# Optimization experiments

Measured on AMD Instinct MI355X. Metric: run time of the kernel, lower is better.

## Reference

```python
import jax, jax.numpy as jnp
import numpy as np

N = 50000   # nodes
E = 500000  # edges
DIN = 128
DOUT = 128
H = 8       # mulhead
DH = DOUT // H
L = 2       # layers per branch
NC = 7      # emotion classes
EPS = 1e-9  # BatchNorm eps from source


def _bn(x):
    # BatchNorm1d in train mode, gamma=1/beta=0 at init
    m = x.mean(axis=0)
    v = x.var(axis=0)
    return (x - m) * jax.lax.rsqrt(v + EPS)


def _gat_forward(f, row, col, vals, Ws, bs, Wn, bn, As, An):
    for i in range(L):
        hs = jax.nn.relu(jnp.einsum('nd,hdk->nhk', f, Ws[i]) + bs[i])  # [N,H,DH]
        hn = jax.nn.relu(jnp.einsum('nd,hdk->nhk', f, Wn[i]) + bn[i])  # [N,H,DH]
        ats = jax.nn.leaky_relu(jnp.einsum('nhk,hk->nh', hs, As[i]), negative_slope=0.2)  # [N,H]
        # NOTE: source computes attention_neigh from f_self (faithful)
        atn = jax.nn.leaky_relu(jnp.einsum('nhk,hk->nh', hs, An[i]), negative_slope=0.2)  # [N,H]
        e = (ats[row] + atn[col]) * vals[:, None]            # [E,H] per-edge attention
        msg = e[:, :, None] * hn[col]                        # [E,H,DH] gather + weight
        agg = jax.ops.segment_sum(msg, row, num_segments=N)  # [N,H,DH] scatter-add (sparse mm)
        f = _bn(agg.reshape(N, H * DH))                      # concat heads + norm
    return f


def _gcn_forward(f, row, col, vals, W, b):
    for i in range(L):
        h = f @ W[i] + b[i]                                  # [N,DOUT]
        agg = jax.ops.segment_sum(vals[:, None] * h[col], row, num_segments=N)
        f = _bn(jax.nn.relu(agg))
    return f


def setup_inputs() -> dict:
    key = jax.random.key(0)
    ks = jax.random.split(key, 24)
    inp = {}
    inp['f_in'] = jax.random.normal(ks[0], (N, DIN), jnp.float32)
    inp['edge_row'] = jax.random.randint(ks[1], (E,), 0, N, jnp.int32)
    inp['edge_col'] = jax.random.randint(ks[2], (E,), 0, N, jnp.int32)
    inp['vals_gat'] = jax.random.uniform(ks[3], (E,), jnp.float32)
    inp['vals_uttr'] = jax.random.uniform(ks[4], (E,), jnp.float32)
    inp['vals_past'] = jax.random.uniform(ks[5], (E,), jnp.float32)
    inp['vals_futr'] = jax.random.uniform(ks[6], (E,), jnp.float32)
    s = 0.05
    # GAT params (stacked over [layer, head]); layer0 in=DIN, later in=DOUT (equal here)
    inp['gat_Ws'] = jax.random.normal(ks[7], (L, H, DIN, DH), jnp.float32) * s
    inp['gat_bs'] = jnp.zeros((L, H, DH), jnp.float32)
    inp['gat_Wn'] = jax.random.normal(ks[8], (L, H, DIN, DH), jnp.float32) * s
    inp['gat_bn'] = jnp.zeros((L, H, DH), jnp.float32)
    inp['gat_as'] = jnp.ones((L, H, DH), jnp.float32)  # init ones per source
    inp['gat_an'] = jnp.ones((L, H, DH), jnp.float32)
    # three vanilla GCN branches
    inp['W_uttr'] = jax.random.normal(ks[9], (L, DIN, DOUT), jnp.float32) * s
    inp['b_uttr'] = jnp.zeros((L, DOUT), jnp.float32)
    inp['W_past'] = jax.random.normal(ks[10], (L, DIN, DOUT), jnp.float32) * s
    inp['b_past'] = jnp.zeros((L, DOUT), jnp.float32)
    inp['W_futr'] = jax.random.normal(ks[11], (L, DIN, DOUT), jnp.float32) * s
    inp['b_futr'] = jnp.zeros((L, DOUT), jnp.float32)
    # self perceptron + classifier
    inp['W_self'] = jax.random.normal(ks[12], (DIN, DOUT), jnp.float32) * s
    inp['b_self'] = jnp.zeros((DOUT,), jnp.float32)
    inp['W_cls'] = jax.random.normal(ks[13], (5 * DOUT, NC), jnp.float32) * s
    inp['b_cls'] = jnp.zeros((NC,), jnp.float32)
    return inp


def reference(f_in, edge_row, edge_col, vals_gat, vals_uttr, vals_past, vals_futr,
              gat_Ws, gat_bs, gat_Wn, gat_bn, gat_as, gat_an,
              W_uttr, b_uttr, W_past, b_past, W_futr, b_futr,
              W_self, b_self, W_cls, b_cls):
    o_gat = _gat_forward(f_in, edge_row, edge_col, vals_gat,
                         gat_Ws, gat_bs, gat_Wn, gat_bn, gat_as, gat_an)
    o_uttr = _gcn_forward(f_in, edge_row, edge_col, vals_uttr, W_uttr, b_uttr)
    o_past = _gcn_forward(f_in, edge_row, edge_col, vals_past, W_past, b_past)
    o_futr = _gcn_forward(f_in, edge_row, edge_col, vals_futr, W_futr, b_futr)
    o_self = _bn(jax.nn.relu(f_in @ W_self + b_self))
    f = jnp.concatenate([o_gat, o_uttr, o_past, o_futr, o_self], axis=1)  # [N,640]
    return f @ W_cls + b_cls  # classifier: act=False, plain linear
```

## Files before the change

### kernel.cpp

```cpp
#include <hip/hip_runtime.h>
#include <hip/hip_bf16.h>


#define NN 50000
#define NE 500000
#define DD 128
#define NH 8
#define DHD 16
#define NCLS 7
#define SCAN_B 196

typedef __attribute__((ext_vector_type(8))) short short8;
typedef __attribute__((ext_vector_type(4))) float f32x4;

__device__ __forceinline__ unsigned short f2bf(float x) {
    unsigned int u = __float_as_uint(x);
    unsigned int r = (u + 0x7fffu + ((u >> 16) & 1u)) >> 16;
    return (unsigned short)r;
}
__device__ __forceinline__ unsigned int pack2bf(float lo, float hi) {
    return (unsigned int)f2bf(lo) | ((unsigned int)f2bf(hi) << 16);
}
__device__ __forceinline__ float bflo(unsigned int u) { return __uint_as_float(u << 16); }
__device__ __forceinline__ float bfhi(unsigned int u) { return __uint_as_float(u & 0xffff0000u); }


__global__ void count_kernel(const int* __restrict__ row, int* __restrict__ cnt) {
    int e = blockIdx.x * 256 + threadIdx.x;
    if (e < NE) atomicAdd(&cnt[row[e]], 1);
}

__global__ __launch_bounds__(256) void scan1_kernel(const int* __restrict__ cnt,
                                                    int* __restrict__ pre,
                                                    int* __restrict__ bsum) {
    __shared__ int s[256];
    int t = threadIdx.x;
    int i = blockIdx.x * 256 + t;
    int v = (i < NN) ? cnt[i] : 0;
    s[t] = v;
    __syncthreads();
    for (int off = 1; off < 256; off <<= 1) {
        int u = (t >= off) ? s[t - off] : 0;
        __syncthreads();
        s[t] += u;
        __syncthreads();
    }
    if (i < NN) pre[i] = s[t] - v;
    if (t == 255) bsum[blockIdx.x] = s[255];
}

__global__ __launch_bounds__(256) void scan2_kernel(const int* __restrict__ bsum,
                                                    int* __restrict__ boff) {
    __shared__ int s[256];
    int t = threadIdx.x;
    int v = (t < SCAN_B) ? bsum[t] : 0;
    s[t] = v;
    __syncthreads();
    for (int off = 1; off < 256; off <<= 1) {
        int u = (t >= off) ? s[t - off] : 0;
        __syncthreads();
        s[t] += u;
        __syncthreads();
    }
    boff[t] = s[t] - v;
    if (t == 255) boff[256] = s[255];
}

__global__ __launch_bounds__(256) void scan3_kernel(const int* __restrict__ pre,
                                                    const int* __restrict__ boff,
                                                    int* __restrict__ row_ptr,
                                                    int* __restrict__ fill) {
    int t = threadIdx.x;
    int i = blockIdx.x * 256 + t;
    if (i < NN) {
        int v = pre[i] + boff[blockIdx.x];
        row_ptr[i] = v;
        fill[i] = v;
    }
    if (blockIdx.x == 0 && t == 0) row_ptr[NN] = boff[256];
}

__global__ void scatter_kernel(const int* __restrict__ row, const int* __restrict__ col,
                               const float* __restrict__ vg, const float* __restrict__ vu,
                               const float* __restrict__ vp, const float* __restrict__ vf,
                               int* __restrict__ fill, int4* __restrict__ ed) {
    int e = blockIdx.x * 256 + threadIdx.x;
    if (e >= NE) return;
    int r = row[e];
    int pos = atomicAdd(&fill[r], 1);
    ed[2 * pos] = make_int4(col[e], __float_as_int(vg[e]), __float_as_int(vu[e]),
                            __float_as_int(vp[e]));
    ed[2 * pos + 1] = make_int4(__float_as_int(vf[e]), 0, 0, 0);
}


__global__ __launch_bounds__(256) void tobf16_kernel(const float* __restrict__ x,
                                                     short* __restrict__ y) {
    int idx = blockIdx.x * 256 + threadIdx.x;
    if (idx >= NN * DD / 8) return;
    float4 a = ((const float4*)x)[idx * 2];
    float4 b = ((const float4*)x)[idx * 2 + 1];
    uint4 o;
    o.x = pack2bf(a.x, a.y);
    o.y = pack2bf(a.z, a.w);
    o.z = pack2bf(b.x, b.y);
    o.w = pack2bf(b.z, b.w);
    *(uint4*)(y + (size_t)idx * 8) = o;
}


struct WPrepArgs {
    const float* src[11];
};

__global__ __launch_bounds__(256) void wprep_kernel(WPrepArgs a, short* __restrict__ out) {
    int idx = blockIdx.x * 256 + threadIdx.x;
    if (idx >= 11 * DD * DD) return;
    int w = idx >> 14;
    int r = idx & 16383;
    int n = r >> 7, k = r & 127;
    const float* W = a.src[w];
    float v = (w < 4) ? W[(size_t)((n >> 4) * DD + k) * DHD + (n & 15)] : W[(size_t)k * DD + n];
    out[idx] = (short)f2bf(v);
}


template <bool RELU_OUT, bool RS, int STATS>
__global__ __launch_bounds__(256) void mfma_mm(const short* __restrict__ A,
                                               const short* __restrict__ Wt,
                                               const float* __restrict__ bias,
                                               const float* __restrict__ rs,
                                               float* __restrict__ stats_out,
                                               float* __restrict__ C) {
    __shared__ short As[64 * DD];
    int t = threadIdx.x;
    int r0 = blockIdx.x * 64;
    {
        int srow = t >> 2;
        int sk0 = (t & 3) * 32;
        int grow = r0 + srow;
#pragma unroll
        for (int j = 0; j < 4; ++j) {
            int k0 = sk0 + j * 8;
            short8 frag = {0, 0, 0, 0, 0, 0, 0, 0};
            if (grow < NN) frag = *(const short8*)(A + (size_t)grow * DD + k0);
            int byte = srow * 256 + k0 * 2;
            byte ^= (srow & 7) << 4;
            *(short8*)((char*)As + byte) = frag;
        }
    }
    __syncthreads();

    int w = t >> 6, l = t & 63;
    int c0 = w * 32;
    int lr = l & 15, lg = l >> 4;
    f32x4 acc[4][2] = {};

#pragma unroll
    for (int s = 0; s < 4; ++s) {
        short8 af[4];
#pragma unroll
        for (int f = 0; f < 4; ++f) {
            int rr = f * 16 + lr;
            int byte = rr * 256 + (s * 32 + lg * 8) * 2;
            byte ^= (rr & 7) << 4;
            af[f] = *(const short8*)((const char*)As + byte);
        }
#pragma unroll
        for (int g = 0; g < 2; ++g) {
            int col = c0 + g * 16 + lr;
            short8 bf = *(const short8*)&Wt[(size_t)col * DD + s * 32 + lg * 8];
#pragma unroll
            for (int f = 0; f < 4; ++f)
                acc[f][g] = __builtin_amdgcn_mfma_f32_16x16x32_bf16(af[f], bf, acc[f][g], 0, 0, 0);
        }
    }

    float rsv[4][4];
    if (RS) {
#pragma unroll
        for (int f = 0; f < 4; ++f)
#pragma unroll
            for (int i = 0; i < 4; ++i) {
                int row = r0 + f * 16 + lg * 4 + i;
                rsv[f][i] = (row < NN) ? rs[row] : 0.f;
            }
    }
    float sA[2] = {0.f, 0.f}, qA[2] = {0.f, 0.f};
#pragma unroll
    for (int g = 0; g < 2; ++g) {
        int col = c0 + g * 16 + lr;
        float b = bias[col];
#pragma unroll
        for (int f = 0; f < 4; ++f) {
#pragma unroll
            for (int i = 0; i < 4; ++i) {
                int row = r0 + f * 16 + lg * 4 + i;
                float o = acc[f][g][i] + (RS ? rsv[f][i] * b : b);
                if (RELU_OUT) o = fmaxf(o, 0.f);
                if (row < NN) {
                    C[(size_t)row * DD + col] = o;
                    if (STATS) {
                        float v = (STATS == 2) ? fmaxf(o, 0.f) : o;
                        sA[g] += v;
                        qA[g] += v * v;
                    }
                }
            }
        }
    }
    if (STATS) {
#pragma unroll
        for (int g = 0; g < 2; ++g) {
            sA[g] += __shfl_xor(sA[g], 16);
            sA[g] += __shfl_xor(sA[g], 32);
            qA[g] += __shfl_xor(qA[g], 16);
            qA[g] += __shfl_xor(qA[g], 32);
        }
        if (lg == 0) {
#pragma unroll
            for (int g = 0; g < 2; ++g) {
                int col = c0 + g * 16 + lr;
                atomicAdd(&stats_out[col], sA[g]);
                atomicAdd(&stats_out[DD + col], qA[g]);
            }
        }
    }
}


template <int PRE>
__global__ __launch_bounds__(256) void mfma_mm_pair(const void* __restrict__ Av,
                                                    const short* __restrict__ Wt1,
                                                    const short* __restrict__ Wt2,
                                                    const float* __restrict__ b1,
                                                    const float* __restrict__ b2,
                                                    const float* __restrict__ a_se,
                                                    const float* __restrict__ a_ne,
                                                    const float* __restrict__ stats_in,
                                                    short* __restrict__ out2,
                                                    float* __restrict__ ats_o,
                                                    float* __restrict__ atn_o) {
    __shared__ short As[64 * DD];
    __shared__ float mS[DD], sS[DD];
    int t = threadIdx.x;
    int r0 = blockIdx.x * 64;

    if (PRE == 1) {
        if (t < DD) {
            const float inv_n = 1.0f / (float)NN;
            float m = stats_in[t] * inv_n;
            float var = stats_in[DD + t] * inv_n - m * m;
            mS[t] = m;
            sS[t] = rsqrtf(var + 1e-9f);
        }
        __syncthreads();
    }
    {
        int srow = t >> 2;
        int sk0 = (t & 3) * 32;
        int grow = r0 + srow;
#pragma unroll
        for (int j = 0; j < 4; ++j) {
            int k0 = sk0 + j * 8;
            short8 frag = {0, 0, 0, 0, 0, 0, 0, 0};
            if (grow < NN) {
                if (PRE == 0) {
                    frag = *(const short8*)((const short*)Av + (size_t)grow * DD + k0);
                } else {
                    const float* Ar = (const float*)Av + (size_t)grow * DD;
                    float4 v0 = *(const float4*)(Ar + k0);
                    float4 v1 = *(const float4*)(Ar + k0 + 4);
                    float vv[8] = {v0.x, v0.y, v0.z, v0.w, v1.x, v1.y, v1.z, v1.w};
#pragma unroll
                    for (int e = 0; e < 8; ++e)
                        frag[e] = (short)f2bf((vv[e] - mS[k0 + e]) * sS[k0 + e]);
                }
            }
            int byte = srow * 256 + k0 * 2;
            byte ^= (srow & 7) << 4;
            *(short8*)((char*)As + byte) = frag;
        }
    }
    __syncthreads();

    int w = t >> 6, l = t & 63;
    int c0 = w * 32;
    int lr = l & 15, lg = l >> 4;
    f32x4 acc1[4][2] = {}, acc2[4][2] = {};

#pragma unroll
    for (int s = 0; s < 4; ++s) {
        short8 af[4];
#pragma unroll
        for (int f = 0; f < 4; ++f) {
            int rr = f * 16 + lr;
            int byte = rr * 256 + (s * 32 + lg * 8) * 2;
            byte ^= (rr & 7) << 4;
            af[f] = *(const short8*)((const char*)As + byte);
        }
#pragma unroll
        for (int g = 0; g < 2; ++g) {
            int col = c0 + g * 16 + lr;
            short8 bfa = *(const short8*)&Wt1[(size_t)col * DD + s * 32 + lg * 8];
            short8 bfb = *(const short8*)&Wt2[(size_t)col * DD + s * 32 + lg * 8];
#pragma unroll
            for (int f = 0; f < 4; ++f) {
                acc1[f][g] = __builtin_amdgcn_mfma_f32_16x16x32_bf16(af[f], bfa, acc1[f][g], 0, 0, 0);
                acc2[f][g] = __builtin_amdgcn_mfma_f32_16x16x32_bf16(af[f], bfb, acc2[f][g], 0, 0, 0);
            }
        }
    }
#pragma unroll
    for (int g = 0; g < 2; ++g) {
        int colc = c0 + g * 16 + lr;
        float bb1 = b1[colc], bb2 = b2[colc];
        float asv = a_se[colc], anv = a_ne[colc];
        int h = (c0 >> 4) + g;
#pragma unroll
        for (int f = 0; f < 4; ++f) {
#pragma unroll
            for (int i = 0; i < 4; ++i) {
                int row = r0 + f * 16 + lg * 4 + i;
                float o1 = fmaxf(acc1[f][g][i] + bb1, 0.f);
                float o2 = fmaxf(acc2[f][g][i] + bb2, 0.f);
                if (row < NN) out2[(size_t)row * DD + colc] = (short)f2bf(o2);
                float ds = o1 * asv, dn = o1 * anv;
                ds += __shfl_xor(ds, 1);
                dn += __shfl_xor(dn, 1);
                ds += __shfl_xor(ds, 2);
                dn += __shfl_xor(dn, 2);
                ds += __shfl_xor(ds, 4);
                dn += __shfl_xor(dn, 4);
                ds += __shfl_xor(ds, 8);
                dn += __shfl_xor(dn, 8);
                if (lr == 0 && row < NN) {
                    ats_o[row * NH + h] = ds > 0.f ? ds : 0.2f * ds;
                    atn_o[row * NH + h] = dn > 0.f ? dn : 0.2f * dn;
                }
            }
        }
    }
}


__global__ __launch_bounds__(256) void spmm_fusedA(
    const short* __restrict__ hnb, const short* __restrict__ fbf, const float* __restrict__ ats,
    const float* __restrict__ atn, const int4* __restrict__ ed, const int* __restrict__ row_ptr,
    float* __restrict__ aggG, short* __restrict__ zu, short* __restrict__ zp,
    short* __restrict__ zf, float* __restrict__ rs_all) {
    int r = __builtin_amdgcn_readfirstlane((blockIdx.x * 256 + threadIdx.x) >> 6);
    int lane = threadIdx.x & 63;
    if (r >= NN) return;
    int hh = lane >> 3;
    float a_s = ats[r * NH + hh];
    int start = row_ptr[r], end = row_ptr[r + 1];
    float2 ag = {0.f, 0.f}, au = {0.f, 0.f}, ap = {0.f, 0.f}, af2 = {0.f, 0.f};
    float su = 0.f, sp = 0.f, sf = 0.f;
    int j = start;
    for (; j + 2 <= end; j += 2) {
        int4 a0 = ed[2 * j], b0 = ed[2 * j + 1];
        int4 a1 = ed[2 * j + 2], b1 = ed[2 * j + 3];
        int cA = a0.x, cB = a1.x;
        float at0 = atn[cA * NH + hh], at1 = atn[cB * NH + hh];
        unsigned int g0 = *(const unsigned int*)(hnb + (size_t)cA * DD + lane * 2);
        unsigned int f0 = *(const unsigned int*)(fbf + (size_t)cA * DD + lane * 2);
        unsigned int g1 = *(const unsigned int*)(hnb + (size_t)cB * DD + lane * 2);
        unsigned int f1 = *(const unsigned int*)(fbf + (size_t)cB * DD + lane * 2);
        {
            float vg = __int_as_float(a0.y), vu = __int_as_float(a0.z);
            float vp = __int_as_float(a0.w), vf = __int_as_float(b0.x);
            float e = (a_s + at0) * vg;
            float glo = bflo(g0), ghi = bfhi(g0), flo = bflo(f0), fhi = bfhi(f0);
            ag.x += e * glo;  ag.y += e * ghi;
            au.x += vu * flo; au.y += vu * fhi;
            ap.x += vp * flo; ap.y += vp * fhi;
            af2.x += vf * flo; af2.y += vf * fhi;
            su += vu; sp += vp; sf += vf;
        }
        {
            float vg = __int_as_float(a1.y), vu = __int_as_float(a1.z);
            float vp = __int_as_float(a1.w), vf = __int_as_float(b1.x);
            float e = (a_s + at1) * vg;
            float glo = bflo(g1), ghi = bfhi(g1), flo = bflo(f1), fhi = bfhi(f1);
            ag.x += e * glo;  ag.y += e * ghi;
            au.x += vu * flo; au.y += vu * fhi;
            ap.x += vp * flo; ap.y += vp * fhi;
            af2.x += vf * flo; af2.y += vf * fhi;
            su += vu; sp += vp; sf += vf;
        }
    }
    if (j < end) {
        int4 a0 = ed[2 * j], b0 = ed[2 * j + 1];
        int cA = a0.x;
        float at0 = atn[cA * NH + hh];
        unsigned int g0 = *(const unsigned int*)(hnb + (size_t)cA * DD + lane * 2);
        unsigned int f0 = *(const unsigned int*)(fbf + (size_t)cA * DD + lane * 2);
        float vg = __int_as_float(a0.y), vu = __int_as_float(a0.z);
        float vp = __int_as_float(a0.w), vf = __int_as_float(b0.x);
        float e = (a_s + at0) * vg;
        float glo = bflo(g0), ghi = bfhi(g0), flo = bflo(f0), fhi = bfhi(f0);
        ag.x += e * glo;  ag.y += e * ghi;
        au.x += vu * flo; au.y += vu * fhi;
        ap.x += vp * flo; ap.y += vp * fhi;
        af2.x += vf * flo; af2.y += vf * fhi;
        su += vu; sp += vp; sf += vf;
    }
    size_t o = (size_t)r * DD + lane * 2;
    *(float2*)&aggG[o] = ag;
    *(unsigned int*)(zu + o) = pack2bf(au.x, au.y);
    *(unsigned int*)(zp + o) = pack2bf(ap.x, ap.y);
    *(unsigned int*)(zf + o) = pack2bf(af2.x, af2.y);
    if (lane == 0) {
        rs_all[r] = su;
        rs_all[NN + r] = sp;
        rs_all[2 * NN + r] = sf;
    }
}


__global__ __launch_bounds__(256) void spmm_gat_kernel(const short* __restrict__ hnb,
                                                       const float* __restrict__ ats,
                                                       const float* __restrict__ atn,
                                                       const int4* __restrict__ ed,
                                                       const int* __restrict__ row_ptr,
                                                       float* __restrict__ agg) {
    int r = __builtin_amdgcn_readfirstlane((blockIdx.x * 256 + threadIdx.x) >> 6);
    int lane = threadIdx.x & 63;
    if (r >= NN) return;
    int hh = lane >> 3;
    float a_s = ats[r * NH + hh];
    int start = row_ptr[r], end = row_ptr[r + 1];
    float2 acc = {0.f, 0.f};
    int j = start;
    for (; j + 2 <= end; j += 2) {
        int4 a0 = ed[2 * j];
        int4 a1 = ed[2 * j + 2];
        int cA = a0.x, cB = a1.x;
        float at0 = atn[cA * NH + hh], at1 = atn[cB * NH + hh];
        unsigned int g0 = *(const unsigned int*)(hnb + (size_t)cA * DD + lane * 2);
        unsigned int g1 = *(const unsigned int*)(hnb + (size_t)cB * DD + lane * 2);
        float e0 = (a_s + at0) * __int_as_float(a0.y);
        float e1 = (a_s + at1) * __int_as_float(a1.y);
        acc.x += e0 * bflo(g0) + e1 * bflo(g1);
        acc.y += e0 * bfhi(g0) + e1 * bfhi(g1);
    }
    if (j < end) {
        int4 a0 = ed[2 * j];
        int cA = a0.x;
        float at0 = atn[cA * NH + hh];
        unsigned int g0 = *(const unsigned int*)(hnb + (size_t)cA * DD + lane * 2);
        float e0 = (a_s + at0) * __int_as_float(a0.y);
        acc.x += e0 * bflo(g0);
        acc.y += e0 * bfhi(g0);
    }
    *(float2*)&agg[(size_t)r * DD + lane * 2] = acc;
}


__global__ __launch_bounds__(256) void spmm_fusedC(const short* __restrict__ f1u,
                                                   const short* __restrict__ f1p,
                                                   const short* __restrict__ f1f,
                                                   const int4* __restrict__ ed,
                                                   const int* __restrict__ row_ptr,
                                                   short* __restrict__ z1u,
                                                   short* __restrict__ z1p,
                                                   short* __restrict__ z1f) {
    int r = __builtin_amdgcn_readfirstlane((blockIdx.x * 256 + threadIdx.x) >> 6);
    int lane = threadIdx.x & 63;
    if (r >= NN) return;
    int start = row_ptr[r], end = row_ptr[r + 1];
    float2 au = {0.f, 0.f}, ap = {0.f, 0.f}, af2 = {0.f, 0.f};
    int j = start;
    for (; j + 2 <= end; j += 2) {
        int4 a0 = ed[2 * j], b0 = ed[2 * j + 1];
        int4 a1 = ed[2 * j + 2], b1 = ed[2 * j + 3];
        int cA = a0.x, cB = a1.x;
        unsigned int u0 = *(const unsigned int*)(f1u + (size_t)cA * DD + lane * 2);
        unsigned int p0 = *(const unsigned int*)(f1p + (size_t)cA * DD + lane * 2);
        unsigned int q0 = *(const unsigned int*)(f1f + (size_t)cA * DD + lane * 2);
        unsigned int u1 = *(const unsigned int*)(f1u + (size_t)cB * DD + lane * 2);
        unsigned int p1 = *(const unsigned int*)(f1p + (size_t)cB * DD + lane * 2);
        unsigned int q1 = *(const unsigned int*)(f1f + (size_t)cB * DD + lane * 2);
        float vu0 = __int_as_float(a0.z), vp0 = __int_as_float(a0.w), vf0 = __int_as_float(b0.x);
        float vu1 = __int_as_float(a1.z), vp1 = __int_as_float(a1.w), vf1 = __int_as_float(b1.x);
        au.x += vu0 * bflo(u0) + vu1 * bflo(u1);
        au.y += vu0 * bfhi(u0) + vu1 * bfhi(u1);
        ap.x += vp0 * bflo(p0) + vp1 * bflo(p1);
        ap.y += vp0 * bfhi(p0) + vp1 * bfhi(p1);
        af2.x += vf0 * bflo(q0) + vf1 * bflo(q1);
        af2.y += vf0 * bfhi(q0) + vf1 * bfhi(q1);
    }
    if (j < end) {
        int4 a0 = ed[2 * j], b0 = ed[2 * j + 1];
        int cA = a0.x;
        unsigned int u0 = *(const unsigned int*)(f1u + (size_t)cA * DD + lane * 2);
        unsigned int p0 = *(const unsigned int*)(f1p + (size_t)cA * DD + lane * 2);
        unsigned int q0 = *(const unsigned int*)(f1f + (size_t)cA * DD + lane * 2);
        float vu0 = __int_as_float(a0.z), vp0 = __int_as_float(a0.w), vf0 = __int_as_float(b0.x);
        au.x += vu0 * bflo(u0);
        au.y += vu0 * bfhi(u0);
        ap.x += vp0 * bflo(p0);
        ap.y += vp0 * bfhi(p0);
        af2.x += vf0 * bflo(q0);
        af2.y += vf0 * bfhi(q0);
    }
    size_t o = (size_t)r * DD + lane * 2;
    *(unsigned int*)(z1u + o) = pack2bf(au.x, au.y);
    *(unsigned int*)(z1p + o) = pack2bf(ap.x, ap.y);
    *(unsigned int*)(z1f + o) = pack2bf(af2.x, af2.y);
}


__global__ __launch_bounds__(256) void bn_stats_kernel(const float* __restrict__ x,
                                                       float* __restrict__ stats) {
    int c = threadIdx.x & 127;
    int sub = threadIdx.x >> 7;
    int rows_per_block = (NN + gridDim.x - 1) / gridDim.x;
    int rbeg = blockIdx.x * rows_per_block;
    int rend = min(rbeg + rows_per_block, NN);
    float s = 0.f, q = 0.f;
    for (int r = rbeg + sub; r < rend; r += 2) {
        float v = x[(size_t)r * DD + c];
        s += v;
        q += v * v;
    }
    atomicAdd(&stats[c], s);
    atomicAdd(&stats[DD + c], q);
}


__global__ __launch_bounds__(256) void bnapply_bf16_kernel(const float* __restrict__ h,
                                                           const float* __restrict__ stats,
                                                           short* __restrict__ outb) {
    __shared__ float mS[DD], sS[DD];
    int t = threadIdx.x;
    if (t < DD) {
        const float inv_n = 1.0f / (float)NN;
        float m = stats[t] * inv_n;
        float var = stats[DD + t] * inv_n - m * m;
        mS[t] = m;
        sS[t] = rsqrtf(var + 1e-9f);
    }
    __syncthreads();
    int idx = blockIdx.x * 256 + t;
    if (idx >= NN * DD / 8) return;
    int c0 = (idx & 15) * 8;
    float4 a = ((const float4*)h)[idx * 2];
    float4 b = ((const float4*)h)[idx * 2 + 1];
    float vv[8] = {a.x, a.y, a.z, a.w, b.x, b.y, b.z, b.w};
#pragma unroll
    for (int e = 0; e < 8; ++e) vv[e] = (fmaxf(vv[e], 0.f) - mS[c0 + e]) * sS[c0 + e];
    uint4 o;
    o.x = pack2bf(vv[0], vv[1]);
    o.y = pack2bf(vv[2], vv[3]);
    o.z = pack2bf(vv[4], vv[5]);
    o.w = pack2bf(vv[6], vv[7]);
    *(uint4*)(outb + (size_t)idx * 8) = o;
}


template <int PRE, bool FIRST>
__global__ __launch_bounds__(256) void cls_acc_kernel(const float* __restrict__ o,
                                                      const float* __restrict__ Wc,
                                                      const float* __restrict__ stats,
                                                      const float* __restrict__ b_cls,
                                                      float* __restrict__ out) {
    __shared__ float Wl[DD * NCLS];
    __shared__ float mS[DD], sS[DD];
    int t = threadIdx.x;
    for (int i = t; i < DD * NCLS; i += 256) Wl[i] = Wc[i];
    if (PRE && t < DD) {
        const float inv_n = 1.0f / (float)NN;
        float m = stats[t] * inv_n;
        float var = stats[DD + t] * inv_n - m * m;
        mS[t] = m;
        sS[t] = rsqrtf(var + 1e-9f);
    }
    __syncthreads();
    int n = blockIdx.x * 256 + t;
    if (n >= NN) return;
    float acc[NCLS] = {};
    const float4* orow = (const float4*)(o + (size_t)n * DD);
    for (int k4 = 0; k4 < DD / 4; ++k4) {
        float4 v = orow[k4];
#pragma unroll
        for (int kk = 0; kk < 4; ++kk) {
            int k = k4 * 4 + kk;
            float a = ((const float*)&v)[kk];
            if (PRE == 2) a = fmaxf(a, 0.f);
            if (PRE) a = (a - mS[k]) * sS[k];
#pragma unroll
            for (int c = 0; c < NCLS; ++c) acc[c] += a * Wl[k * NCLS + c];
        }
    }
#pragma unroll
    for (int c = 0; c < NCLS; ++c) {
        if (FIRST)
            out[n * NCLS + c] = acc[c] + b_cls[c];
        else
            out[n * NCLS + c] += acc[c];
    }
}


extern "C" void kernel_launch(void* const* d_in, const int* in_sizes, int n_in, void* d_out,
                              int out_size, void* d_ws, size_t ws_size, hipStream_t stream) {
    const float* f_in = (const float*)d_in[0];
    const int* edge_row = (const int*)d_in[1];
    const int* edge_col = (const int*)d_in[2];
    const float* vals_gat = (const float*)d_in[3];
    const float* vals_uttr = (const float*)d_in[4];
    const float* vals_past = (const float*)d_in[5];
    const float* vals_futr = (const float*)d_in[6];
    const float* gat_Ws = (const float*)d_in[7];
    const float* gat_bs = (const float*)d_in[8];
    const float* gat_Wn = (const float*)d_in[9];
    const float* gat_bn = (const float*)d_in[10];
    const float* gat_as = (const float*)d_in[11];
    const float* gat_an = (const float*)d_in[12];
    const float* W_uttr = (const float*)d_in[13];
    const float* b_uttr = (const float*)d_in[14];
    const float* W_past = (const float*)d_in[15];
    const float* b_past = (const float*)d_in[16];
    const float* W_futr = (const float*)d_in[17];
    const float* b_futr = (const float*)d_in[18];
    const float* W_self = (const float*)d_in[19];
    const float* b_self = (const float*)d_in[20];
    const float* W_cls = (const float*)d_in[21];
    const float* b_cls = (const float*)d_in[22];
    float* out = (float*)d_out;

    char* ws = (char*)d_ws;
    size_t off = 0;
    auto alloc = [&](size_t bytes) -> void* {
        void* p = ws + off;
        off = (off + bytes + 255) & ~(size_t)255;
        return p;
    };
    float* stats_all = (float*)alloc(9 * 2 * DD * 4);
    int* cnt = (int*)alloc((size_t)NN * 4);
    float* tmp1 = (float*)alloc((size_t)NN * DD * 4);
    float* bufA = (float*)alloc((size_t)NN * DD * 4);
    short* fbf = (short*)alloc((size_t)NN * DD * 2);
    short* hnb = (short*)alloc((size_t)NN * DD * 2);
    short* z0u = (short*)alloc((size_t)NN * DD * 2);
    short* z0p = (short*)alloc((size_t)NN * DD * 2);
    short* z0f = (short*)alloc((size_t)NN * DD * 2);
    float* rs_all = (float*)alloc((size_t)3 * NN * 4);
    float* ats_b = (float*)alloc((size_t)NN * NH * 4);
    float* atn_b = (float*)alloc((size_t)NN * NH * 4);
    short* Wt_all = (short*)alloc((size_t)11 * DD * DD * 2);
    int* row_ptr = (int*)alloc((size_t)(NN + 1) * 4);
    int* fill = (int*)alloc((size_t)NN * 4);
    int* pre_b = (int*)alloc((size_t)NN * 4);
    int* bsum = (int*)alloc((size_t)SCAN_B * 4);
    int* boff = (int*)alloc((size_t)257 * 4);
    int4* ed = (int4*)alloc((size_t)NE * 32);

    auto stats = [&](int s) { return stats_all + (size_t)s * 2 * DD; };
    auto Wt = [&](int w) { return Wt_all + (size_t)w * DD * DD; };
    short* z0[3] = {z0u, z0p, z0f};
    short* z1[3] = {hnb, (short*)bufA, (short*)bufA + (size_t)NN * DD};

    const int gE = (NE + 255) / 256;
    const int gMM = (NN + 63) / 64;
    const int gSP = (NN + 3) / 4;
    const int gCA = (NN + 255) / 256;
    const int gBF = (NN * DD / 8 + 255) / 256;

    hipMemsetAsync(stats_all, 0, 9 * 2 * DD * 4 + (size_t)NN * 4, stream);

    count_kernel<<<gE, 256, 0, stream>>>(edge_row, cnt);
    scan1_kernel<<<SCAN_B, 256, 0, stream>>>(cnt, pre_b, bsum);
    scan2_kernel<<<1, 256, 0, stream>>>(bsum, boff);
    scan3_kernel<<<SCAN_B, 256, 0, stream>>>(pre_b, boff, row_ptr, fill);
    scatter_kernel<<<gE, 256, 0, stream>>>(edge_row, edge_col, vals_gat, vals_uttr, vals_past,
                                           vals_futr, fill, ed);

    tobf16_kernel<<<gBF, 256, 0, stream>>>(f_in, fbf);

    WPrepArgs wa;
    wa.src[0] = gat_Ws;
    wa.src[1] = gat_Wn;
    wa.src[2] = gat_Ws + (size_t)DD * DD;
    wa.src[3] = gat_Wn + (size_t)DD * DD;
    wa.src[4] = W_uttr;
    wa.src[5] = W_uttr + (size_t)DD * DD;
    wa.src[6] = W_past;
    wa.src[7] = W_past + (size_t)DD * DD;
    wa.src[8] = W_futr;
    wa.src[9] = W_futr + (size_t)DD * DD;
    wa.src[10] = W_self;
    wprep_kernel<<<(11 * DD * DD + 255) / 256, 256, 0, stream>>>(wa, Wt_all);

    mfma_mm<true, false, 1><<<gMM, 256, 0, stream>>>(fbf, Wt(10), b_self, nullptr, stats(8), tmp1);
    cls_acc_kernel<1, true><<<gCA, 256, 0, stream>>>(tmp1, W_cls + (size_t)4 * DD * NCLS,
                                                     stats(8), b_cls, out);

    mfma_mm_pair<0><<<gMM, 256, 0, stream>>>(fbf, Wt(0), Wt(1), gat_bs, gat_bn, gat_as, gat_an,
                                             nullptr, hnb, ats_b, atn_b);
    spmm_fusedA<<<gSP, 256, 0, stream>>>(hnb, fbf, ats_b, atn_b, ed, row_ptr, bufA, z0u, z0p,
                                         z0f, rs_all);
    bn_stats_kernel<<<256, 256, 0, stream>>>(bufA, stats(0));
    mfma_mm_pair<1><<<gMM, 256, 0, stream>>>(bufA, Wt(2), Wt(3), gat_bs + DD, gat_bn + DD,
                                             gat_as + DD, gat_an + DD, stats(0), hnb, ats_b,
                                             atn_b);
    spmm_gat_kernel<<<gSP, 256, 0, stream>>>(hnb, ats_b, atn_b, ed, row_ptr, bufA);
    bn_stats_kernel<<<256, 256, 0, stream>>>(bufA, stats(1));
    cls_acc_kernel<1, false><<<gCA, 256, 0, stream>>>(bufA, W_cls, stats(1), b_cls, out);

    const float* bb[3] = {b_uttr, b_past, b_futr};
    for (int br = 0; br < 3; ++br) {
        int w0 = 4 + br * 2;
        int s0 = 2 + br * 2;
        mfma_mm<false, true, 2><<<gMM, 256, 0, stream>>>(z0[br], Wt(w0), bb[br],
                                                         rs_all + (size_t)br * NN, stats(s0),
                                                         tmp1);
        bnapply_bf16_kernel<<<gBF, 256, 0, stream>>>(tmp1, stats(s0), z0[br]);
    }
    spmm_fusedC<<<gSP, 256, 0, stream>>>(z0u, z0p, z0f, ed, row_ptr, z1[0], z1[1], z1[2]);
    for (int br = 0; br < 3; ++br) {
        int w0 = 4 + br * 2;
        int s0 = 2 + br * 2;
        mfma_mm<false, true, 2><<<gMM, 256, 0, stream>>>(z1[br], Wt(w0 + 1), bb[br] + DD,
                                                         rs_all + (size_t)br * NN, stats(s0 + 1),
                                                         tmp1);
        cls_acc_kernel<2, false><<<gCA, 256, 0, stream>>>(
            tmp1, W_cls + (size_t)(DD + DD * br) * NCLS, stats(s0 + 1), b_cls, out);
    }
}
```

Before: 664.5 us.

## Fold GCN BatchNorm into next-layer weights and fuse GAT/GCN sparse aggregation

Layer-0 GCN batchnorm is no longer applied elementwise. Its mean and scale are folded into the layer-1 weights and a bias correction scaled by the row sums, computed by a small new kernel. This allows the layer-1 GAT aggregation and the three GCN aggregations to run in a single sparse pass. The three branch matmuls are batched into one launch with bf16 outputs, removing fp32 intermediates and the bnapply passes. The risk is extra bf16 rounding on unnormalized activations and more register pressure in the fused spmm.

```diff
diff --git a/kernel.cpp b/kernel.cpp
--- a/kernel.cpp
+++ b/kernel.cpp
@@ -125,13 +125,40 @@
 }
 
 
-template <bool RELU_OUT, bool RS, int STATS>
-__global__ __launch_bounds__(256) void mfma_mm(const short* __restrict__ A,
-                                               const short* __restrict__ Wt,
-                                               const float* __restrict__ bias,
-                                               const float* __restrict__ rs,
-                                               float* __restrict__ stats_out,
-                                               float* __restrict__ C) {
+struct WFixArgs {
+    const float* W1[3];
+    const float* b1[3];
+    const float* stats[3];
+};
+
+__global__ __launch_bounds__(256) void wfix_kernel(WFixArgs a, short* __restrict__ wt_out,
+                                                   float* __restrict__ bfix) {
+    int idx = blockIdx.x * 256 + threadIdx.x;
+    if (idx >= 3 * DD) return;
+    int br = idx >> 7, n = idx & 127;
+    const float* st = a.stats[br];
+    const float* W = a.W1[br];
+    const float inv_n = 1.0f / (float)NN;
+    float accb = 0.f;
+    short* wo = wt_out + (size_t)br * DD * DD + (size_t)n * DD;
+#pragma unroll 4
+    for (int k = 0; k < DD; ++k) {
+        float m = st[k] * inv_n;
+        float var = st[DD + k] * inv_n - m * m;
+        float s = rsqrtf(var + 1e-9f);
+        float w = W[(size_t)k * DD + n];
+        wo[k] = (short)f2bf(s * w);
+        accb += m * s * w;
+    }
+    bfix[idx] = a.b1[br][n] - accb;
+}
+
+
+__global__ __launch_bounds__(256) void mfma_mm_self(const short* __restrict__ A,
+                                                    const short* __restrict__ Wt,
+                                                    const float* __restrict__ bias,
+                                                    float* __restrict__ stats_out,
+                                                    float* __restrict__ C) {
     __shared__ short As[64 * DD];
     int t = threadIdx.x;
     int r0 = blockIdx.x * 64;
@@ -150,12 +177,10 @@
         }
     }
     __syncthreads();
-
     int w = t >> 6, l = t & 63;
     int c0 = w * 32;
     int lr = l & 15, lg = l >> 4;
     f32x4 acc[4][2] = {};
-
 #pragma unroll
     for (int s = 0; s < 4; ++s) {
         short8 af[4];
@@ -175,57 +200,140 @@
                 acc[f][g] = __builtin_amdgcn_mfma_f32_16x16x32_bf16(af[f], bf, acc[f][g], 0, 0, 0);
         }
     }
-
-    float rsv[4][4];
-    if (RS) {
-#pragma unroll
-        for (int f = 0; f < 4; ++f)
-#pragma unroll
-            for (int i = 0; i < 4; ++i) {
-                int row = r0 + f * 16 + lg * 4 + i;
-                rsv[f][i] = (row < NN) ? rs[row] : 0.f;
-            }
-    }
     float sA[2] = {0.f, 0.f}, qA[2] = {0.f, 0.f};
 #pragma unroll
     for (int g = 0; g < 2; ++g) {
         int col = c0 + g * 16 + lr;
         float b = bias[col];
 #pragma unroll
-        for (int f = 0; f < 4; ++f) {
+        for (int f = 0; f < 4; ++f)
 #pragma unroll
             for (int i = 0; i < 4; ++i) {
                 int row = r0 + f * 16 + lg * 4 + i;
-                float o = acc[f][g][i] + (RS ? rsv[f][i] * b : b);
-                if (RELU_OUT) o = fmaxf(o, 0.f);
                 if (row < NN) {
+                    float o = fmaxf(acc[f][g][i] + b, 0.f);
                     C[(size_t)row * DD + col] = o;
-                    if (STATS) {
-                        float v = (STATS == 2) ? fmaxf(o, 0.f) : o;
-                        sA[g] += v;
-                        qA[g] += v * v;
-                    }
+                    sA[g] += o;
+                    qA[g] += o * o;
                 }
             }
-        }
-    }
-    if (STATS) {
+    }
+#pragma unroll
+    for (int g = 0; g < 2; ++g) {
+        sA[g] += __shfl_xor(sA[g], 16);
+        sA[g] += __shfl_xor(sA[g], 32);
+        qA[g] += __shfl_xor(qA[g], 16);
+        qA[g] += __shfl_xor(qA[g], 32);
+    }
+    if (lg == 0)
 #pragma unroll
         for (int g = 0; g < 2; ++g) {
-            sA[g] += __shfl_xor(sA[g], 16);
-            sA[g] += __shfl_xor(sA[g], 32);
-            qA[g] += __shfl_xor(qA[g], 16);
-            qA[g] += __shfl_xor(qA[g], 32);
-        }
-        if (lg == 0) {
-#pragma unroll
-            for (int g = 0; g < 2; ++g) {
-                int col = c0 + g * 16 + lr;
-                atomicAdd(&stats_out[col], sA[g]);
-                atomicAdd(&stats_out[DD + col], qA[g]);
+            int col = c0 + g * 16 + lr;
+            atomicAdd(&stats_out[col], sA[g]);
+            atomicAdd(&stats_out[DD + col], qA[g]);
+        }
+}
+
+
+struct MMB {
+    const short* A[3];
+    const short* W[3];
+    const float* bias[3];
+    const float* rs[3];
+    float* stats[3];
+    short* C[3];
+};
+
+__global__ __launch_bounds__(256) void mfma_mm_gcn(MMB m) {
+    int br = blockIdx.y;
+    const short* A = m.A[br];
+    const short* Wt = m.W[br];
+    const float* bias = m.bias[br];
+    const float* rs = m.rs[br];
+    float* stats_out = m.stats[br];
+    short* C = m.C[br];
+
+    __shared__ short As[64 * DD];
+    int t = threadIdx.x;
+    int r0 = blockIdx.x * 64;
+    {
+        int srow = t >> 2;
+        int sk0 = (t & 3) * 32;
+        int grow = r0 + srow;
+#pragma unroll
+        for (int j = 0; j < 4; ++j) {
+            int k0 = sk0 + j * 8;
+            short8 frag = {0, 0, 0, 0, 0, 0, 0, 0};
+            if (grow < NN) frag = *(const short8*)(A + (size_t)grow * DD + k0);
+            int byte = srow * 256 + k0 * 2;
+            byte ^= (srow & 7) << 4;
+            *(short8*)((char*)As + byte) = frag;
+        }
+    }
+    __syncthreads();
+    int w = t >> 6, l = t & 63;
+    int c0 = w * 32;
+    int lr = l & 15, lg = l >> 4;
+    f32x4 acc[4][2] = {};
+#pragma unroll
+    for (int s = 0; s < 4; ++s) {
+        short8 af[4];
+#pragma unroll
+        for (int f = 0; f < 4; ++f) {
+            int rr = f * 16 + lr;
+            int byte = rr * 256 + (s * 32 + lg * 8) * 2;
+            byte ^= (rr & 7) << 4;
+            af[f] = *(const short8*)((const char*)As + byte);
+        }
+#pragma unroll
+        for (int g = 0; g < 2; ++g) {
+            int col = c0 + g * 16 + lr;
+            short8 bf = *(const short8*)&Wt[(size_t)col * DD + s * 32 + lg * 8];
+#pragma unroll
+            for (int f = 0; f < 4; ++f)
+                acc[f][g] = __builtin_amdgcn_mfma_f32_16x16x32_bf16(af[f], bf, acc[f][g], 0, 0, 0);
+        }
+    }
+    float rsv[4][4];
+#pragma unroll
+    for (int f = 0; f < 4; ++f)
+#pragma unroll
+        for (int i = 0; i < 4; ++i) {
+            int row = r0 + f * 16 + lg * 4 + i;
+            rsv[f][i] = (row < NN) ? rs[row] : 0.f;
+        }
+    float sA[2] = {0.f, 0.f}, qA[2] = {0.f, 0.f};
+#pragma unroll
+    for (int g = 0; g < 2; ++g) {
+        int col = c0 + g * 16 + lr;
+        float b = bias[col];
+#pragma unroll
+        for (int f = 0; f < 4; ++f)
+#pragma unroll
+            for (int i = 0; i < 4; ++i) {
+                int row = r0 + f * 16 + lg * 4 + i;
+                if (row < NN) {
+                    float o = fmaxf(acc[f][g][i] + rsv[f][i] * b, 0.f);
+                    C[(size_t)row * DD + col] = (short)f2bf(o);
+                    sA[g] += o;
+                    qA[g] += o * o;
+                }
             }
-        }
-    }
+    }
+#pragma unroll
+    for (int g = 0; g < 2; ++g) {
+        sA[g] += __shfl_xor(sA[g], 16);
+        sA[g] += __shfl_xor(sA[g], 32);
+        qA[g] += __shfl_xor(qA[g], 16);
+        qA[g] += __shfl_xor(qA[g], 32);
+    }
+    if (lg == 0)
+#pragma unroll
+        for (int g = 0; g < 2; ++g) {
+            int col = c0 + g * 16 + lr;
+            atomicAdd(&stats_out[col], sA[g]);
+            atomicAdd(&stats_out[DD + col], qA[g]);
+        }
 }
 
 
@@ -245,7 +353,6 @@
     __shared__ float mS[DD], sS[DD];
     int t = threadIdx.x;
     int r0 = blockIdx.x * 64;
-
     if (PRE == 1) {
         if (t < DD) {
             const float inv_n = 1.0f / (float)NN;
@@ -283,12 +390,10 @@
         }
     }
     __syncthreads();
-
     int w = t >> 6, l = t & 63;
     int c0 = w * 32;
     int lr = l & 15, lg = l >> 4;
     f32x4 acc1[4][2] = {}, acc2[4][2] = {};
-
 #pragma unroll
     for (int s = 0; s < 4; ++s) {
         short8 af[4];
@@ -318,7 +423,7 @@
         float asv = a_se[colc], anv = a_ne[colc];
         int h = (c0 >> 4) + g;
 #pragma unroll
-        for (int f = 0; f < 4; ++f) {
+        for (int f = 0; f < 4; ++f)
 #pragma unroll
             for (int i = 0; i < 4; ++i) {
                 int row = r0 + f * 16 + lg * 4 + i;
@@ -339,7 +444,6 @@
                     atn_o[row * NH + h] = dn > 0.f ? dn : 0.2f * dn;
                 }
             }
-        }
     }
 }
 
@@ -419,71 +523,39 @@
 }
 
 
-__global__ __launch_bounds__(256) void spmm_gat_kernel(const short* __restrict__ hnb,
-                                                       const float* __restrict__ ats,
-                                                       const float* __restrict__ atn,
-                                                       const int4* __restrict__ ed,
-                                                       const int* __restrict__ row_ptr,
-                                                       float* __restrict__ agg) {
+__global__ __launch_bounds__(256) void spmm_fusedB(
+    const short* __restrict__ hnb, const short* __restrict__ y0u, const short* __restrict__ y0p,
+    const short* __restrict__ y0f, const float* __restrict__ ats, const float* __restrict__ atn,
+    const int4* __restrict__ ed, const int* __restrict__ row_ptr, float* __restrict__ aggG,
+    short* __restrict__ z1u, short* __restrict__ z1p, short* __restrict__ z1f) {
     int r = __builtin_amdgcn_readfirstlane((blockIdx.x * 256 + threadIdx.x) >> 6);
     int lane = threadIdx.x & 63;
     if (r >= NN) return;
     int hh = lane >> 3;
     float a_s = ats[r * NH + hh];
     int start = row_ptr[r], end = row_ptr[r + 1];
-    float2 acc = {0.f, 0.f};
-    int j = start;
-    for (; j + 2 <= end; j += 2) {
-        int4 a0 = ed[2 * j];
-        int4 a1 = ed[2 * j + 2];
-        int cA = a0.x, cB = a1.x;
-        float at0 = atn[cA * NH + hh], at1 = atn[cB * NH + hh];
-        unsigned int g0 = *(const unsigned int*)(hnb + (size_t)cA * DD + lane * 2);
-        unsigned int g1 = *(const unsigned int*)(hnb + (size_t)cB * DD + lane * 2);
-        float e0 = (a_s + at0) * __int_as_float(a0.y);
-        float e1 = (a_s + at1) * __int_as_float(a1.y);
-        acc.x += e0 * bflo(g0) + e1 * bflo(g1);
-        acc.y += e0 * bfhi(g0) + e1 * bfhi(g1);
-    }
-    if (j < end) {
-        int4 a0 = ed[2 * j];
-        int cA = a0.x;
-        float at0 = atn[cA * NH + hh];
-        unsigned int g0 = *(const unsigned int*)(hnb + (size_t)cA * DD + lane * 2);
-        float e0 = (a_s + at0) * __int_as_float(a0.y);
-        acc.x += e0 * bflo(g0);
-        acc.y += e0 * bfhi(g0);
-    }
-    *(float2*)&agg[(size_t)r * DD + lane * 2] = acc;
-}
-
-
-__global__ __launch_bounds__(256) void spmm_fusedC(const short* __restrict__ f1u,
-                                                   const short* __restrict__ f1p,
-                                                   const short* __restrict__ f1f,
-                                                   const int4* __restrict__ ed,
-                                                   const int* __restrict__ row_ptr,
-                                                   short* __restrict__ z1u,
-                                                   short* __restrict__ z1p,
-                                                   short* __restrict__ z1f) {
-    int r = __builtin_amdgcn_readfirstlane((blockIdx.x * 256 + threadIdx.x) >> 6);
-    int lane = threadIdx.x & 63;
-    if (r >= NN) return;
-    int start = row_ptr[r], end = row_ptr[r + 1];
-    float2 au = {0.f, 0.f}, ap = {0.f, 0.f}, af2 = {0.f, 0.f};
+    float2 ag = {0.f, 0.f}, au = {0.f, 0.f}, ap = {0.f, 0.f}, af2 = {0.f, 0.f};
     int j = start;
     for (; j + 2 <= end; j += 2) {
         int4 a0 = ed[2 * j], b0 = ed[2 * j + 1];
         int4 a1 = ed[2 * j + 2], b1 = ed[2 * j + 3];
         int cA = a0.x, cB = a1.x;
-        unsigned int u0 = *(const unsigned int*)(f1u + (size_t)cA * DD + lane * 2);
-        unsigned int p0 = *(const unsigned int*)(f1p + (size_t)cA * DD + lane * 2);
-        unsigned int q0 = *(const unsigned int*)(f1f + (size_t)cA * DD + lane * 2);
-        unsigned int u1 = *(const unsigned int*)(f1u + (size_t)cB * DD + lane * 2);
-        unsigned int p1 = *(const unsigned int*)(f1p + (size_t)cB * DD + lane * 2);
-        unsigned int q1 = *(const unsigned int*)(f1f + (size_t)cB * DD + lane * 2);
+        float at0 = atn[cA * NH + hh], at1 = atn[cB * NH + hh];
+        size_t oA = (size_t)cA * DD + lane * 2, oB = (size_t)cB * DD + lane * 2;
+        unsigned int g0 = *(const unsigned int*)(hnb + oA);
+        unsigned int u0 = *(const unsigned int*)(y0u + oA);
+        unsigned int p0 = *(const unsigned int*)(y0p + oA);
+        unsigned int q0 = *(const unsigned int*)(y0f + oA);
+        unsigned int g1 = *(const unsigned int*)(hnb + oB);
+        unsigned int u1 = *(const unsigned int*)(y0u + oB);
+        unsigned int p1 = *(const unsigned int*)(y0p + oB);
+        unsigned int q1 = *(const unsigned int*)(y0f + oB);
+        float e0 = (a_s + at0) * __int_as_float(a0.y);
+        float e1 = (a_s + at1) * __int_as_float(a1.y);
         float vu0 = __int_as_float(a0.z), vp0 = __int_as_float(a0.w), vf0 = __int_as_float(b0.x);
         float vu1 = __int_as_float(a1.z), vp1 = __int_as_float(a1.w), vf1 = __int_as_float(b1.x);
+        ag.x += e0 * bflo(g0) + e1 * bflo(g1);
+        ag.y += e0 * bfhi(g0) + e1 * bfhi(g1);
         au.x += vu0 * bflo(u0) + vu1 * bflo(u1);
         au.y += vu0 * bfhi(u0) + vu1 * bfhi(u1);
         ap.x += vp0 * bflo(p0) + vp1 * bflo(p1);
@@ -494,10 +566,16 @@
     if (j < end) {
         int4 a0 = ed[2 * j], b0 = ed[2 * j + 1];
         int cA = a0.x;
-        unsigned int u0 = *(const unsigned int*)(f1u + (size_t)cA * DD + lane * 2);
-        unsigned int p0 = *(const unsigned int*)(f1p + (size_t)cA * DD + lane * 2);
-        unsigned int q0 = *(const unsigned int*)(f1f + (size_t)cA * DD + lane * 2);
+        float at0 = atn[cA * NH + hh];
+        size_t oA = (size_t)cA * DD + lane * 2;
+        unsigned int g0 = *(const unsigned int*)(hnb + oA);
+        unsigned int u0 = *(const unsigned int*)(y0u + oA);
+        unsigned int p0 = *(const unsigned int*)(y0p + oA);
+        unsigned int q0 = *(const unsigned int*)(y0f + oA);
+        float e0 = (a_s + at0) * __int_as_float(a0.y);
         float vu0 = __int_as_float(a0.z), vp0 = __int_as_float(a0.w), vf0 = __int_as_float(b0.x);
+        ag.x += e0 * bflo(g0);
+        ag.y += e0 * bfhi(g0);
         au.x += vu0 * bflo(u0);
         au.y += vu0 * bfhi(u0);
         ap.x += vp0 * bflo(p0);
@@ -506,6 +584,7 @@
         af2.y += vf0 * bfhi(q0);
     }
     size_t o = (size_t)r * DD + lane * 2;
+    *(float2*)&aggG[o] = ag;
     *(unsigned int*)(z1u + o) = pack2bf(au.x, au.y);
     *(unsigned int*)(z1p + o) = pack2bf(ap.x, ap.y);
     *(unsigned int*)(z1f + o) = pack2bf(af2.x, af2.y);
@@ -530,38 +609,8 @@
 }
 
 
-__global__ __launch_bounds__(256) void bnapply_bf16_kernel(const float* __restrict__ h,
-                                                           const float* __restrict__ stats,
-                                                           short* __restrict__ outb) {
-    __shared__ float mS[DD], sS[DD];
-    int t = threadIdx.x;
-    if (t < DD) {
-        const float inv_n = 1.0f / (float)NN;
-        float m = stats[t] * inv_n;
-        float var = stats[DD + t] * inv_n - m * m;
-        mS[t] = m;
-        sS[t] = rsqrtf(var + 1e-9f);
-    }
-    __syncthreads();
-    int idx = blockIdx.x * 256 + t;
-    if (idx >= NN * DD / 8) return;
-    int c0 = (idx & 15) * 8;
-    float4 a = ((const float4*)h)[idx * 2];
-    float4 b = ((const float4*)h)[idx * 2 + 1];
-    float vv[8] = {a.x, a.y, a.z, a.w, b.x, b.y, b.z, b.w};
-#pragma unroll
-    for (int e = 0; e < 8; ++e) vv[e] = (fmaxf(vv[e], 0.f) - mS[c0 + e]) * sS[c0 + e];
-    uint4 o;
-    o.x = pack2bf(vv[0], vv[1]);
-    o.y = pack2bf(vv[2], vv[3]);
-    o.z = pack2bf(vv[4], vv[5]);
-    o.w = pack2bf(vv[6], vv[7]);
-    *(uint4*)(outb + (size_t)idx * 8) = o;
-}
-
-
-template <int PRE, bool FIRST>
-__global__ __launch_bounds__(256) void cls_acc_kernel(const float* __restrict__ o,
+template <int PRE, bool FIRST, bool BF16IN>
+__global__ __launch_bounds__(256) void cls_acc_kernel(const void* __restrict__ ov,
                                                       const float* __restrict__ Wc,
                                                       const float* __restrict__ stats,
                                                       const float* __restrict__ b_cls,
@@ -581,17 +630,35 @@
     int n = blockIdx.x * 256 + t;
     if (n >= NN) return;
     float acc[NCLS] = {};
-    const float4* orow = (const float4*)(o + (size_t)n * DD);
-    for (int k4 = 0; k4 < DD / 4; ++k4) {
-        float4 v = orow[k4];
-#pragma unroll
-        for (int kk = 0; kk < 4; ++kk) {
-            int k = k4 * 4 + kk;
-            float a = ((const float*)&v)[kk];
-            if (PRE == 2) a = fmaxf(a, 0.f);
-            if (PRE) a = (a - mS[k]) * sS[k];
-#pragma unroll
-            for (int c = 0; c < NCLS; ++c) acc[c] += a * Wl[k * NCLS + c];
+    if (BF16IN) {
+        const uint4* orow = (const uint4*)((const short*)ov + (size_t)n * DD);
+        for (int k8 = 0; k8 < DD / 8; ++k8) {
+            uint4 v = orow[k8];
+            float vv[8] = {bflo(v.x), bfhi(v.x), bflo(v.y), bfhi(v.y),
+                           bflo(v.z), bfhi(v.z), bflo(v.w), bfhi(v.w)};
+#pragma unroll
+            for (int kk = 0; kk < 8; ++kk) {
+                int k = k8 * 8 + kk;
+                float a = vv[kk];
+                if (PRE == 2) a = fmaxf(a, 0.f);
+                if (PRE) a = (a - mS[k]) * sS[k];
+#pragma unroll
+                for (int c = 0; c < NCLS; ++c) acc[c] += a * Wl[k * NCLS + c];
+            }
+        }
+    } else {
+        const float4* orow = (const float4*)((const float*)ov + (size_t)n * DD);
+        for (int k4 = 0; k4 < DD / 4; ++k4) {
+            float4 v = orow[k4];
+#pragma unroll
+            for (int kk = 0; kk < 4; ++kk) {
+                int k = k4 * 4 + kk;
+                float a = ((const float*)&v)[kk];
+                if (PRE == 2) a = fmaxf(a, 0.f);
+                if (PRE) a = (a - mS[k]) * sS[k];
+#pragma unroll
+                for (int c = 0; c < NCLS; ++c) acc[c] += a * Wl[k * NCLS + c];
+            }
         }
     }
 #pragma unroll
@@ -650,7 +717,8 @@
     float* rs_all = (float*)alloc((size_t)3 * NN * 4);
     float* ats_b = (float*)alloc((size_t)NN * NH * 4);
     float* atn_b = (float*)alloc((size_t)NN * NH * 4);
-    short* Wt_all = (short*)alloc((size_t)11 * DD * DD * 2);
+    short* Wt_all = (short*)alloc((size_t)14 * DD * DD * 2);
+    float* bfix = (float*)alloc((size_t)3 * DD * 4);
     int* row_ptr = (int*)alloc((size_t)(NN + 1) * 4);
     int* fill = (int*)alloc((size_t)NN * 4);
     int* pre_b = (int*)alloc((size_t)NN * 4);
@@ -660,8 +728,6 @@
 
     auto stats = [&](int s) { return stats_all + (size_t)s * 2 * DD; };
     auto Wt = [&](int w) { return Wt_all + (size_t)w * DD * DD; };
-    short* z0[3] = {z0u, z0p, z0f};
-    short* z1[3] = {hnb, (short*)bufA, (short*)bufA + (size_t)NN * DD};
 
     const int gE = (NE + 255) / 256;
     const int gMM = (NN + 63) / 64;
@@ -694,9 +760,9 @@
     wa.src[10] = W_self;
     wprep_kernel<<<(11 * DD * DD + 255) / 256, 256, 0, stream>>>(wa, Wt_all);
 
-    mfma_mm<true, false, 1><<<gMM, 256, 0, stream>>>(fbf, Wt(10), b_self, nullptr, stats(8), tmp1);
-    cls_acc_kernel<1, true><<<gCA, 256, 0, stream>>>(tmp1, W_cls + (size_t)4 * DD * NCLS,
-                                                     stats(8), b_cls, out);
+    mfma_mm_self<<<gMM, 256, 0, stream>>>(fbf, Wt(10), b_self, stats(8), tmp1);
+    cls_acc_kernel<1, true, false><<<gCA, 256, 0, stream>>>(tmp1, W_cls + (size_t)4 * DD * NCLS,
+                                                            stats(8), b_cls, out);
 
     mfma_mm_pair<0><<<gMM, 256, 0, stream>>>(fbf, Wt(0), Wt(1), gat_bs, gat_bn, gat_as, gat_an,
                                              nullptr, hnb, ats_b, atn_b);
@@ -706,27 +772,50 @@
     mfma_mm_pair<1><<<gMM, 256, 0, stream>>>(bufA, Wt(2), Wt(3), gat_bs + DD, gat_bn + DD,
                                              gat_as + DD, gat_an + DD, stats(0), hnb, ats_b,
                                              atn_b);
-    spmm_gat_kernel<<<gSP, 256, 0, stream>>>(hnb, ats_b, atn_b, ed, row_ptr, bufA);
+
+    const float* bb[3] = {b_uttr, b_past, b_futr};
+    const float* Worig[3] = {W_uttr, W_past, W_futr};
+    MMB m0;
+    short* z0a[3] = {z0u, z0p, z0f};
+    for (int br = 0; br < 3; ++br) {
+        m0.A[br] = z0a[br];
+        m0.W[br] = Wt(4 + br * 2);
+        m0.bias[br] = bb[br];
+        m0.rs[br] = rs_all + (size_t)br * NN;
+        m0.stats[br] = stats(2 + br);
+        m0.C[br] = z0a[br];
+    }
+    mfma_mm_gcn<<<dim3(gMM, 3), 256, 0, stream>>>(m0);
+
+    WFixArgs wf;
+    for (int br = 0; br < 3; ++br) {
+        wf.W1[br] = Worig[br] + (size_t)DD * DD;
+        wf.b1[br] = bb[br] + DD;
+        wf.stats[br] = stats(2 + br);
+    }
+    wfix_kernel<<<2, 256, 0, stream>>>(wf, Wt(11), bfix);
+
+    short* z1u = fbf;
+    short* z1p = (short*)tmp1;
+    short* z1f = (short*)tmp1 + (size_t)NN * DD;
+    spmm_fusedB<<<gSP, 256, 0, stream>>>(hnb, z0u, z0p, z0f, ats_b, atn_b, ed, row_ptr, bufA,
+                                         z1u, z1p, z1f);
     bn_stats_kernel<<<256, 256, 0, stream>>>(bufA, stats(1));
-    cls_acc_kernel<1, false><<<gCA, 256, 0, stream>>>(bufA, W_cls, stats(1), b_cls, out);
-
-    const float* bb[3] = {b_uttr, b_past, b_futr};
+    cls_acc_kernel<1, false, false><<<gCA, 256, 0, stream>>>(bufA, W_cls, stats(1), b_cls, out);
+
+    MMB m1;
+    short* z1a[3] = {z1u, z1p, z1f};
     for (int br = 0; br < 3; ++br) {
-        int w0 = 4 + br * 2;
-        int s0 = 2 + br * 2;
-        mfma_mm<false, true, 2><<<gMM, 256, 0, stream>>>(z0[br], Wt(w0), bb[br],
-                                                         rs_all + (size_t)br * NN, stats(s0),
-                                                         tmp1);
-        bnapply_bf16_kernel<<<gBF, 256, 0, stream>>>(tmp1, stats(s0), z0[br]);
-    }
-    spmm_fusedC<<<gSP, 256, 0, stream>>>(z0u, z0p, z0f, ed, row_ptr, z1[0], z1[1], z1[2]);
-    for (int br = 0; br < 3; ++br) {
-        int w0 = 4 + br * 2;
-        int s0 = 2 + br * 2;
-        mfma_mm<false, true, 2><<<gMM, 256, 0, stream>>>(z1[br], Wt(w0 + 1), bb[br] + DD,
-                                                         rs_all + (size_t)br * NN, stats(s0 + 1),
-                                                         tmp1);
-        cls_acc_kernel<2, false><<<gCA, 256, 0, stream>>>(
-            tmp1, W_cls + (size_t)(DD + DD * br) * NCLS, stats(s0 + 1), b_cls, out);
-    }
-}
+        m1.A[br] = z1a[br];
+        m1.W[br] = Wt(11 + br);
+        m1.bias[br] = bfix + (size_t)br * DD;
+        m1.rs[br] = rs_all + (size_t)br * NN;
+        m1.stats[br] = stats(5 + br);
+        m1.C[br] = z0a[br];
+    }
+    mfma_mm_gcn<<<dim3(gMM, 3), 256, 0, stream>>>(m1);
+
+    for (int br = 0; br < 3; ++br)
+        cls_acc_kernel<1, false, true><<<gCA, 256, 0, stream>>>(
+            z0a[br], W_cls + (size_t)(DD + DD * br) * NCLS, stats(5 + br), b_cls, out);
+}
```

Result: faster. 572.8 us (-13.8%).
